# Kernel tuning notes

Hardware: AMD Instinct MI355X
Metric: run time of the kernel (lower is better)

## Reference

```python
import jax, jax.numpy as jnp
import numpy as np
from math import pi

B, CIN, COUT, H, W, K, STRIDE, PAD = 4, 32, 64, 32, 32, 3, 1, 1


def setup_inputs() -> dict:
    key = jax.random.key(0)
    k1, k2, k3 = jax.random.split(key, 3)
    x = jax.random.normal(k1, (B, CIN, H, W), dtype=jnp.float32)
    probe = jax.random.uniform(k2, (1, CIN, COUT, 1, 1, K, K), dtype=jnp.float32, minval=-pi, maxval=pi)
    out_w = jax.random.uniform(k3, (1, CIN, COUT, 1, 1, K, K), dtype=jnp.float32, minval=-pi, maxval=pi)
    return {"x": x, "probe": probe, "out_w": out_w}


def _patches(x):
    # sliding-window gather, equivalent to x.unfold(2,K,S).unfold(3,K,S)
    p = jax.lax.conv_general_dilated_patches(
        x, filter_shape=(K, K), window_strides=(STRIDE, STRIDE),
        padding=[(PAD, PAD), (PAD, PAD)])  # (B, CIN*K*K, Ho, Wo), channel-major
    b, _, ho, wo = p.shape
    p = p.reshape(b, CIN, K, K, ho, wo)
    return jnp.transpose(p, (0, 1, 4, 5, 2, 3))  # (B, CIN, Ho, Wo, K, K)


def reference(x, probe, out_w):
    pat = _patches(x)[:, :, None]                 # (B, CIN, 1, Ho, Wo, K, K)
    act = jnp.cos(pat - probe) ** 3               # (B, CIN, COUT, Ho, Wo, K, K)
    cw = jnp.cos(out_w).reshape(CIN, COUT, K, K)  # squeeze broadcast dims
    sw = jnp.sin(out_w).reshape(CIN, COUT, K, K)
    out_x = jnp.einsum('cokl,bcohwkl->bohw', cw, act)
    out_y = jnp.einsum('cokl,bcohwkl->bohw', sw, act)
    return jnp.arctan2(out_y, out_x)              # (B, COUT, Ho, Wo)
```

## Files before the change

### kernel.cpp

```cpp
#include <hip/hip_runtime.h>
#include <math.h>


typedef _Float16 half8 __attribute__((ext_vector_type(8)));
typedef float floatx4 __attribute__((ext_vector_type(4)));

#define B_TAP_STRIDE (128 * 256)
#define B_VSTRIDE (9u * 128 * 256)

__global__ __launch_bounds__(256) void ring_prep_b(
    const float* __restrict__ probe, const float* __restrict__ outw,
    char* __restrict__ Bg) {
  int i = blockIdx.x * 256 + threadIdx.x;
  int p = i & 15;
  int n = (i >> 4) & 127;
  int tap = i >> 11;
  int qd = p ^ (n & 7);
  int o = n & 63;
  int xy = n >> 6;
  half8 hi, lo;
#pragma unroll
  for (int hf = 0; hf < 2; ++hf) {
    int c = qd * 2 + hf;
    int idx = (c * 64 + o) * 9 + tap;
    float th = probe[idx];
    float wvv = outw[idx];
    float sth, cth, sw, cw;
    __sincosf(th, &sth, &cth);
    __sincosf(wvv, &sw, &cw);
    float c3 = cth * fmaf(4.0f * cth, cth, -3.0f);
    float s3 = sth * fmaf(-4.0f * sth, sth, 3.0f);
    float m = xy ? sw : cw;
    float v4[4] = {0.75f * m * cth, 0.75f * m * sth, 0.25f * m * c3,
                   0.25f * m * s3};
#pragma unroll
    for (int f = 0; f < 4; ++f) {
      _Float16 hv = (_Float16)v4[f];
      hi[hf * 4 + f] = hv;
      lo[hf * 4 + f] = (_Float16)((v4[f] - (float)hv) * 2048.0f);
    }
  }
  size_t off = (((size_t)tap * 128 + n) * 16 + p) * 16;
  *(half8*)(Bg + off) = hi;
  *(half8*)(Bg + off + B_VSTRIDE) = lo;
}

__global__ __launch_bounds__(256, 2) void ring_mfma(
    const float* __restrict__ x, const char* __restrict__ Bg,
    float* __restrict__ out) {
  __shared__ __align__(16) char sA[27648];
  __shared__ float sEx[512];

  int blk = blockIdx.x;
  int oh = blk & 1;
  int wt = (blk >> 1) & 1;
  int h = (blk >> 2) & 31;
  int b = blk >> 7;
  int tid = threadIdx.x;

  int lane = tid & 63;
  int wv = tid >> 6;
  int n16 = lane & 15;
  int quad = lane >> 4;
  int xy = wv >> 1;
  int og = wv & 1;

  int n_global = xy * 64 + oh * 32 + og * 16 + n16;
  const char* bRow = Bg + (size_t)n_global * 256;
  const char* bRowL = bRow + B_VSTRIDE;
  int bkey = n16 & 7;

  half8 BcH0, BcH1, BcH2, BcH3, BcL0, BcL1, BcL2, BcL3;
  {
    int p0 = ((0 * 4 + quad) ^ bkey) * 16;
    int p1 = ((1 * 4 + quad) ^ bkey) * 16;
    int p2 = ((2 * 4 + quad) ^ bkey) * 16;
    int p3 = ((3 * 4 + quad) ^ bkey) * 16;
    BcH0 = *(const half8*)(bRow + p0);
    BcH1 = *(const half8*)(bRow + p1);
    BcH2 = *(const half8*)(bRow + p2);
    BcH3 = *(const half8*)(bRow + p3);
    BcL0 = *(const half8*)(bRowL + p0);
    BcL1 = *(const half8*)(bRowL + p1);
    BcL2 = *(const half8*)(bRowL + p2);
    BcL3 = *(const half8*)(bRowL + p3);
  }

  for (int u = tid; u < 864; u += 256) {
    int r = u / 288;
    int t = u - r * 288;
    int colidx = t >> 4;
    int p = t & 15;
    int q = p ^ (colidx & 7);
    int hs = h + r - 1;
    int wsx = wt * 16 + colidx - 1;
    bool valid = ((unsigned)hs < 32u) && ((unsigned)wsx < 32u);
    half8 hi, lo;
#pragma unroll
    for (int hf = 0; hf < 2; ++hf) {
      int c = q * 2 + hf;
      float c1 = 1.0f, s1 = 0.0f;
      if (valid) {
        float pv = x[((b * 32 + c) * 32 + hs) * 32 + wsx];
        __sincosf(pv, &s1, &c1);
      }
      float c3 = c1 * fmaf(4.0f * c1, c1, -3.0f);
      float s3 = s1 * fmaf(-4.0f * s1, s1, 3.0f);
      float v4[4] = {c1, s1, c3, s3};
#pragma unroll
      for (int f = 0; f < 4; ++f) {
        _Float16 hv = (_Float16)v4[f];
        hi[hf * 4 + f] = hv;
        lo[hf * 4 + f] = (_Float16)((v4[f] - (float)hv) * 2048.0f);
      }
    }
    *(half8*)(sA + u * 16) = hi;
    *(half8*)(sA + u * 16 + 13824) = lo;
  }

  floatx4 acc0 = {0.f, 0.f, 0.f, 0.f};
  floatx4 acc1 = {0.f, 0.f, 0.f, 0.f};
  floatx4 acc2 = {0.f, 0.f, 0.f, 0.f};

  __syncthreads();

#pragma unroll
  for (int tap = 0; tap < 9; ++tap) {
    half8 BnH0, BnH1, BnH2, BnH3, BnL0, BnL1, BnL2, BnL3;
    if (tap < 8) {
      const char* bn = bRow + (size_t)(tap + 1) * B_TAP_STRIDE;
      const char* bnL = bn + B_VSTRIDE;
      int p0 = ((0 * 4 + quad) ^ bkey) * 16;
      int p1 = ((1 * 4 + quad) ^ bkey) * 16;
      int p2 = ((2 * 4 + quad) ^ bkey) * 16;
      int p3 = ((3 * 4 + quad) ^ bkey) * 16;
      BnH0 = *(const half8*)(bn + p0);
      BnH1 = *(const half8*)(bn + p1);
      BnH2 = *(const half8*)(bn + p2);
      BnH3 = *(const half8*)(bn + p3);
      BnL0 = *(const half8*)(bnL + p0);
      BnL1 = *(const half8*)(bnL + p1);
      BnL2 = *(const half8*)(bnL + p2);
      BnL3 = *(const half8*)(bnL + p3);
    }

    int dk = tap / 3;
    int l = tap - dk * 3;
    int colidx = n16 + l;
    int akey = colidx & 7;
    const char* aH = sA + (dk * 18 + colidx) * 256;
    const char* aL = sA + ((3 + dk) * 18 + colidx) * 256;

#pragma unroll
    for (int ks = 0; ks < 4; ++ks) {
      int pa = ((ks * 4 + quad) ^ akey) * 16;
      half8 Ah = *(const half8*)(aH + pa);
      half8 Al = *(const half8*)(aL + pa);
      half8 Bh = (ks == 0) ? BcH0 : (ks == 1) ? BcH1 : (ks == 2) ? BcH2 : BcH3;
      half8 Bl = (ks == 0) ? BcL0 : (ks == 1) ? BcL1 : (ks == 2) ? BcL2 : BcL3;
      acc0 = __builtin_amdgcn_mfma_f32_16x16x32_f16(Ah, Bh, acc0, 0, 0, 0);
      acc1 = __builtin_amdgcn_mfma_f32_16x16x32_f16(Al, Bh, acc1, 0, 0, 0);
      acc2 = __builtin_amdgcn_mfma_f32_16x16x32_f16(Ah, Bl, acc2, 0, 0, 0);
    }
    BcH0 = BnH0; BcH1 = BnH1; BcH2 = BnH2; BcH3 = BnH3;
    BcL0 = BnL0; BcL1 = BnL1; BcL2 = BnL2; BcL3 = BnL3;
  }

  floatx4 fin = acc0 + (acc1 + acc2) * (1.0f / 2048.0f);

  __syncthreads();
  if (xy == 1) {
#pragma unroll
    for (int r = 0; r < 4; ++r)
      sEx[(og * 16 + n16) * 16 + quad * 4 + r] = fin[r];
  }
  __syncthreads();
  if (xy == 0) {
    int o = oh * 32 + og * 16 + n16;
    float4 res;
    float* rp = (float*)&res;
#pragma unroll
    for (int r = 0; r < 4; ++r) {
      int m = quad * 4 + r;
      float ay = sEx[(og * 16 + n16) * 16 + m];
      rp[r] = atan2f(ay, fin[r]);
    }
    float* dst = out + (((size_t)(b * 64 + o) * 32 + h) * 32 + wt * 16 + quad * 4);
    *(float4*)dst = res;
  }
}

extern "C" void kernel_launch(void* const* d_in, const int* in_sizes, int n_in,
                              void* d_out, int out_size, void* d_ws, size_t ws_size,
                              hipStream_t stream) {
  const float* x = (const float*)d_in[0];
  const float* probe = (const float*)d_in[1];
  const float* outw = (const float*)d_in[2];
  char* Bg = (char*)d_ws;
  float* out = (float*)d_out;

  ring_prep_b<<<72, 256, 0, stream>>>(probe, outw, Bg);
  ring_mfma<<<512, 256, 0, stream>>>(x, Bg, out);
}
```

Measured before the change: 69.78 us.

## Merge two width tiles per block to share halo A-tile staging

Each block now covers a full 32-wide output row using 512 threads (8 waves), instead of two blocks each handling a 16-column half. The shared A tile holds 34 columns, so the halo columns and the sincos work are no longer duplicated across the two width halves, and the grid is halved. In exchange each block uses about 56KB of LDS, which may limit how many blocks fit per CU, and the number of blocks drops to 256.

```diff
diff --git a/kernel.cpp b/kernel.cpp
--- a/kernel.cpp
+++ b/kernel.cpp
@@ -45,55 +45,54 @@
   *(half8*)(Bg + off + B_VSTRIDE) = lo;
 }
 
-__global__ __launch_bounds__(256, 2) void ring_mfma(
+#define AL_OFF 26112
+
+__global__ __launch_bounds__(512, 2) void ring_mfma(
     const float* __restrict__ x, const char* __restrict__ Bg,
     float* __restrict__ out) {
-  __shared__ __align__(16) char sA[27648];
-  __shared__ float sEx[512];
+  __shared__ __align__(16) char sA[52224];
+  __shared__ float sEx[1024];
 
   int blk = blockIdx.x;
   int oh = blk & 1;
-  int wt = (blk >> 1) & 1;
-  int h = (blk >> 2) & 31;
-  int b = blk >> 7;
+  int h = (blk >> 1) & 31;
+  int b = blk >> 6;
   int tid = threadIdx.x;
 
   int lane = tid & 63;
   int wv = tid >> 6;
   int n16 = lane & 15;
   int quad = lane >> 4;
-  int xy = wv >> 1;
+  int wt = wv >> 2;
+  int xy = (wv >> 1) & 1;
   int og = wv & 1;
 
   int n_global = xy * 64 + oh * 32 + og * 16 + n16;
   const char* bRow = Bg + (size_t)n_global * 256;
   const char* bRowL = bRow + B_VSTRIDE;
   int bkey = n16 & 7;
+  int p0 = ((0 * 4 + quad) ^ bkey) * 16;
+  int p1 = ((1 * 4 + quad) ^ bkey) * 16;
+  int p2 = ((2 * 4 + quad) ^ bkey) * 16;
+  int p3 = ((3 * 4 + quad) ^ bkey) * 16;
 
-  half8 BcH0, BcH1, BcH2, BcH3, BcL0, BcL1, BcL2, BcL3;
-  {
-    int p0 = ((0 * 4 + quad) ^ bkey) * 16;
-    int p1 = ((1 * 4 + quad) ^ bkey) * 16;
-    int p2 = ((2 * 4 + quad) ^ bkey) * 16;
-    int p3 = ((3 * 4 + quad) ^ bkey) * 16;
-    BcH0 = *(const half8*)(bRow + p0);
-    BcH1 = *(const half8*)(bRow + p1);
-    BcH2 = *(const half8*)(bRow + p2);
-    BcH3 = *(const half8*)(bRow + p3);
-    BcL0 = *(const half8*)(bRowL + p0);
-    BcL1 = *(const half8*)(bRowL + p1);
-    BcL2 = *(const half8*)(bRowL + p2);
-    BcL3 = *(const half8*)(bRowL + p3);
-  }
+  half8 BcH0 = *(const half8*)(bRow + p0);
+  half8 BcH1 = *(const half8*)(bRow + p1);
+  half8 BcH2 = *(const half8*)(bRow + p2);
+  half8 BcH3 = *(const half8*)(bRow + p3);
+  half8 BcL0 = *(const half8*)(bRowL + p0);
+  half8 BcL1 = *(const half8*)(bRowL + p1);
+  half8 BcL2 = *(const half8*)(bRowL + p2);
+  half8 BcL3 = *(const half8*)(bRowL + p3);
 
-  for (int u = tid; u < 864; u += 256) {
-    int r = u / 288;
-    int t = u - r * 288;
-    int colidx = t >> 4;
-    int p = t & 15;
+  for (int u = tid; u < 1632; u += 512) {
+    int p = u & 15;
+    int t = u >> 4;
+    int colidx = t % 34;
+    int r = t / 34;
     int q = p ^ (colidx & 7);
     int hs = h + r - 1;
-    int wsx = wt * 16 + colidx - 1;
+    int wsx = colidx - 1;
     bool valid = ((unsigned)hs < 32u) && ((unsigned)wsx < 32u);
     half8 hi, lo;
 #pragma unroll
@@ -115,7 +114,7 @@
       }
     }
     *(half8*)(sA + u * 16) = hi;
-    *(half8*)(sA + u * 16 + 13824) = lo;
+    *(half8*)(sA + u * 16 + AL_OFF) = lo;
   }
 
   floatx4 acc0 = {0.f, 0.f, 0.f, 0.f};
@@ -130,10 +129,6 @@
     if (tap < 8) {
       const char* bn = bRow + (size_t)(tap + 1) * B_TAP_STRIDE;
       const char* bnL = bn + B_VSTRIDE;
-      int p0 = ((0 * 4 + quad) ^ bkey) * 16;
-      int p1 = ((1 * 4 + quad) ^ bkey) * 16;
-      int p2 = ((2 * 4 + quad) ^ bkey) * 16;
-      int p3 = ((3 * 4 + quad) ^ bkey) * 16;
       BnH0 = *(const half8*)(bn + p0);
       BnH1 = *(const half8*)(bn + p1);
       BnH2 = *(const half8*)(bn + p2);
@@ -146,10 +141,10 @@
 
     int dk = tap / 3;
     int l = tap - dk * 3;
-    int colidx = n16 + l;
+    int colidx = wt * 16 + n16 + l;
     int akey = colidx & 7;
-    const char* aH = sA + (dk * 18 + colidx) * 256;
-    const char* aL = sA + ((3 + dk) * 18 + colidx) * 256;
+    const char* aH = sA + (dk * 34 + colidx) * 256;
+    const char* aL = aH + AL_OFF;
 
 #pragma unroll
     for (int ks = 0; ks < 4; ++ks) {
@@ -172,7 +167,7 @@
   if (xy == 1) {
 #pragma unroll
     for (int r = 0; r < 4; ++r)
-      sEx[(og * 16 + n16) * 16 + quad * 4 + r] = fin[r];
+      sEx[((wt * 2 + og) * 16 + n16) * 16 + quad * 4 + r] = fin[r];
   }
   __syncthreads();
   if (xy == 0) {
@@ -182,7 +177,7 @@
 #pragma unroll
     for (int r = 0; r < 4; ++r) {
       int m = quad * 4 + r;
-      float ay = sEx[(og * 16 + n16) * 16 + m];
+      float ay = sEx[((wt * 2 + og) * 16 + n16) * 16 + m];
       rp[r] = atan2f(ay, fin[r]);
     }
     float* dst = out + (((size_t)(b * 64 + o) * 32 + h) * 32 + wt * 16 + quad * 4);
@@ -200,5 +195,5 @@
   float* out = (float*)d_out;
 
   ring_prep_b<<<72, 256, 0, stream>>>(probe, outw, Bg);
-  ring_mfma<<<512, 256, 0, stream>>>(x, Bg, out);
+  ring_mfma<<<256, 512, 0, stream>>>(x, Bg, out);
 }
```

Result: no change. 69.87 us (+0.1%).
